# Kernel tuning notes

Measured on AMD Instinct MI355X. Metric: run time of the kernel, lower is better.

## Reference

```python
import jax, jax.numpy as jnp
import numpy as np

T, B, S, V = 50, 64, 400, 50000
D = 512; E = 512; H = 512; A = 512; POOL = 2


def setup_inputs() -> dict:
    key = jax.random.key(0)
    ks = jax.random.split(key, 20)
    def rn(k, shape, s=0.05):
        return jax.random.normal(k, shape, jnp.float32) * s
    return {
        "input_y": jax.random.randint(ks[0], (T, B), 0, V),
        "hidden": rn(ks[1], (1, B, H), 1.0),
        "context": rn(ks[2], (S, B, E), 1.0),
        "src_pad_mask": jnp.zeros((B, S), jnp.float32),
        "init_att": rn(ks[3], (B, E), 1.0),
        "coverage": jnp.zeros((B, S), jnp.float32),
        "global_ctx": rn(ks[4], (B, E), 1.0),
        "emb_W": rn(ks[5], (V, D)).at[0].set(0.0),  # padding_idx=0
        "W_ih": rn(ks[6], (3 * H, D + E)),
        "W_hh": rn(ks[7], (3 * H, H)),
        "b_ih": jnp.zeros((3 * H,), jnp.float32),
        "b_hh": jnp.zeros((3 * H,), jnp.float32),
        "W_pre": rn(ks[8], (E, A)),
        "b_pre": jnp.zeros((A,), jnp.float32),
        "W_q": rn(ks[9], (H + E, A)),
        "W_v": rn(ks[10], (A,)),
        "W_cov": rn(ks[11], (A,)),
        "W_pgen": rn(ks[12], (E + H + D,)),
        "b_pgen": jnp.zeros((), jnp.float32),
        "W_ro": rn(ks[13], (D + H + E + E, H)),
        "b_ro": jnp.zeros((H,), jnp.float32),
    }


def _gru_cell(x, h, W_ih, W_hh, b_ih, b_hh):
    # PyTorch GRUCell gate order: r, z, n
    gi = x @ W_ih.T + b_ih
    gh = h @ W_hh.T + b_hh
    i_r, i_z, i_n = jnp.split(gi, 3, axis=-1)
    h_r, h_z, h_n = jnp.split(gh, 3, axis=-1)
    r = jax.nn.sigmoid(i_r + h_r)
    z = jax.nn.sigmoid(i_z + h_z)
    n = jnp.tanh(i_n + r * h_n)
    return (1.0 - z) * n + z * h


def reference(input_y, hidden, context, src_pad_mask, init_att, coverage, global_ctx,
              emb_W, W_ih, W_hh, b_ih, b_hh, W_pre, b_pre, W_q, W_v, W_cov,
              W_pgen, b_pgen, W_ro, b_ro):
    emb = emb_W[input_y]                      # [T,B,D]
    ctx = jnp.transpose(context, (1, 0, 2))   # [B,S,E]
    precompute = ctx @ W_pre + b_pre          # [B,S,A] (computed once, as in module)
    pad = src_pad_mask > 0.5
    NEG = jnp.float32(-1e18)

    def step(carry, emb_t):
        h, cur_ctx, cov = carry
        x = jnp.concatenate([emb_t, cur_ctx], 1)          # input feed
        h0 = _gru_cell(x, h[0], W_ih, W_hh, b_ih, b_hh)   # layers=1
        h = h.at[0].set(h0)
        output = h0
        # concat attention with coverage
        q = jnp.concatenate([output, global_ctx], 1) @ W_q          # [B,A]
        tmp = jnp.tanh(precompute + q[:, None, :] + cov[..., None] * W_cov)
        energy = tmp @ W_v                                           # [B,S]
        energy = jnp.where(pad, NEG, energy)
        attn = jax.nn.softmax(energy, axis=1)
        cur_ctx = jnp.einsum('bs,bse->be', attn, ctx)
        # pointer-gen
        p_gen = jax.nn.sigmoid(
            jnp.concatenate([cur_ctx, output, emb_t], 1) @ W_pgen + b_pgen)[:, None]
        # readout + maxout (dropout is identity in eval)
        readout = jnp.concatenate([emb_t, output, cur_ctx, global_ctx], 1) @ W_ro + b_ro
        mo = readout.reshape(B, H // POOL, POOL).max(axis=-1)        # [B,H/POOL]
        cov_loss = jnp.sum(jnp.minimum(attn, cov), 1)                # cov_loss_wt=1.0
        next_cov = cov + attn
        return (h, cur_ctx, next_cov), (mo, p_gen, attn, cov_loss)

    (hidden_f, cur_ctx_f, cov_f), (g_out, g_pg, g_attn, cov_losses) = jax.lax.scan(
        step, (hidden, init_att, coverage), emb)
    return (g_out, hidden_f, g_attn[-1], cur_ctx_f, g_pg, g_attn, cov_losses, cov_f)
```

## Files before the change

kernel.cpp:

```cpp
#include <hip/hip_runtime.h>
#include <hip/hip_bf16.h>


#define T_STEPS 50
#define BB 64
#define SS 400

#define O_GOUT 0
#define O_HID 819200
#define O_ATTN_LAST 851968
#define O_CTXF 877568
#define O_PG 910336
#define O_GATTN 913536
#define O_COVL 2193536
#define O_COVF 2196736

typedef __attribute__((ext_vector_type(4))) float f4;
typedef __attribute__((ext_vector_type(8))) short s8v;
typedef __attribute__((ext_vector_type(4))) unsigned u4;

static __device__ __forceinline__ float bf2f(unsigned short u){
  unsigned v = ((unsigned)u) << 16; return __builtin_bit_cast(float, v);
}
static __device__ __forceinline__ unsigned short f2bf(float f){
  unsigned u = __builtin_bit_cast(unsigned, f);
  unsigned r = (u + 0x7FFFu + ((u >> 16) & 1u)) >> 16;
  return (unsigned short)r;
}
static __device__ __forceinline__ float sigmoidf_(float x){ return 1.f/(1.f+__expf(-x)); }
static __device__ __forceinline__ float tanhf_(float x){ float e=__expf(2.f*x); return 1.f - 2.f/(e+1.f); }
static __device__ __forceinline__ float ald32f(const float* p){
  unsigned u = __hip_atomic_load((const unsigned*)p, __ATOMIC_RELAXED, __HIP_MEMORY_SCOPE_AGENT);
  return __builtin_bit_cast(float, u);
}
static __device__ __forceinline__ void ast32f(float* p, float v){
  __hip_atomic_store((unsigned*)p, __builtin_bit_cast(unsigned, v),
                     __ATOMIC_RELAXED, __HIP_MEMORY_SCOPE_AGENT);
}

__global__ void conv_ctx(const float* __restrict__ ctx, unsigned short* __restrict__ out){
  int o = blockIdx.x*256 + threadIdx.x;
  if(o >= SS*BB*512) return;
  int e = o & 511; int b = (o>>9)&63; int s = o>>15;
  out[((b*SS+s)<<9) + e] = f2bf(ctx[o]);
}
__global__ void conv_emb(const int* __restrict__ y, const float* __restrict__ embW,
                         unsigned short* __restrict__ embU){
  int o = blockIdx.x*256+threadIdx.x; if(o>=T_STEPS*BB*512) return;
  int d = o & 511; int i = o>>9;
  embU[o] = f2bf(embW[(long)y[i]*512 + d]);
}
__global__ void conv_rest(const float* __restrict__ W_ih, const float* __restrict__ W_hh,
                          const float* __restrict__ W_pre, const float* __restrict__ W_ro,
                          const float* __restrict__ W_q,
                          const float* __restrict__ hidden, const float* __restrict__ init_att,
                          const float* __restrict__ gctx, const float* __restrict__ coverage,
                          unsigned short* __restrict__ wihbf, unsigned short* __restrict__ wpreT,
                          unsigned short* __restrict__ wroT, unsigned short* __restrict__ Wgru,
                          unsigned short* __restrict__ WqP,
                          float* __restrict__ hrow0, unsigned short* __restrict__ h0bf_init,
                          unsigned short* __restrict__ ctx0bf, float* __restrict__ gctxT,
                          float* __restrict__ cov, unsigned* __restrict__ flags){
  int o = blockIdx.x*256+threadIdx.x;
  if(o < 786432){
    int j = o>>9; int d = o&511;
    wihbf[o] = f2bf(W_ih[(long)j*1024 + d]);
  } else if(o < 1048576){
    int p = o - 786432;
    int a = p>>9; int e = p&511;
    wpreT[p] = f2bf(W_pre[(long)e*512 + a]);
  } else if(o < 2097152){
    int p = o - 1048576;
    int n = p>>11; int k = p&2047;
    wroT[p] = f2bf(W_ro[(long)k*512 + n]);
  } else if(o < 3670016){
    int p = o - 2097152;
    int rg = p >> 13; int rem = p & 8191;
    int ki = rem >> 9; int ln = (rem >> 3) & 63; int e = p & 7;
    int blk = rg/24; int r2 = rg%24; int w = r2/6; int r3 = r2%6; int g = r3>>1; int op = r3&1;
    int rl = ln & 15; int kk = ((ln>>4)<<3) + e;
    int d = blk*64 + w*16 + rl; int j = g*512 + d; int k = ki*32 + kk;
    float v = op ? W_hh[(long)j*512 + k] : W_ih[(long)j*1024 + 512 + k];
    Wgru[p] = f2bf(v);
  } else if(o < 3932160){
    int p = o - 3670016;
    int e = p&7; int ln=(p>>3)&63; int kf=(p>>9)&1; int nrg=(p>>10)&31; int blk=p>>15;
    int n = nrg*16 + (ln&15);
    int k = blk*64 + kf*32 + ((ln>>4)<<3) + e;
    WqP[p] = f2bf(W_q[(long)k*512 + n]);
  } else if(o < 4056128){
    int p = o - 3932160;
    if(p < 32768){ float v = hidden[p]; hrow0[p] = v; h0bf_init[p] = f2bf(v); }
    else if(p < 65536){ int q=p-32768; ctx0bf[q] = f2bf(init_att[q]); }
    else if(p < 98304){ int q=p-65536; int b=q>>9,e=q&511; gctxT[e*64+b]=gctx[q]; }
    else if(p < 123904){ int q=p-98304; cov[q]=coverage[q]; }
    else { int q=p-123904; if(q<64) flags[q]=0u; }
  }
}

template<int OUT_BF16>
__global__ __launch_bounds__(256) void mfma_gemm(
    const unsigned short* __restrict__ Abf, int lda,
    const unsigned short* __restrict__ Bbf, int ldb,
    void* __restrict__ Cp, int ldc, const float* __restrict__ bias, int K)
{
  __shared__ __align__(16) unsigned short Ash[128*40];
  __shared__ __align__(16) unsigned short Bsh[128*40];
  int m0 = blockIdx.x*128, n0 = blockIdx.y*128;
  int tid = threadIdx.x;
  int wid = tid>>6, lane = tid&63;
  int wm = wid>>1, wn = wid&1;
  int lr = lane&15, lg = lane>>4;
  f4 acc[4][4];
  #pragma unroll
  for(int i=0;i<4;i++)
    #pragma unroll
    for(int j=0;j<4;j++) acc[i][j]=(f4)0.f;

  for(int kt=0; kt<K; kt+=32){
    #pragma unroll
    for(int c=0;c<2;c++){
      int flat = tid*16 + c*8;
      int row = flat>>5, col = flat&31;
      const unsigned short* ga = Abf + (long)(m0+row)*lda + kt + col;
      *(uint4*)(&Ash[row*40+col]) = *(const uint4*)ga;
      const unsigned short* gb = Bbf + (long)(n0+row)*ldb + kt + col;
      *(uint4*)(&Bsh[row*40+col]) = *(const uint4*)gb;
    }
    __syncthreads();
    s8v av[4], bv[4];
    #pragma unroll
    for(int mi=0;mi<4;mi++) av[mi] = *(const s8v*)(&Ash[(wm*64+mi*16+lr)*40 + lg*8]);
    #pragma unroll
    for(int ni=0;ni<4;ni++) bv[ni] = *(const s8v*)(&Bsh[(wn*64+ni*16+lr)*40 + lg*8]);
    #pragma unroll
    for(int mi=0;mi<4;mi++)
      #pragma unroll
      for(int ni=0;ni<4;ni++)
        acc[mi][ni] = __builtin_amdgcn_mfma_f32_16x16x32_bf16(av[mi], bv[ni], acc[mi][ni], 0,0,0);
    __syncthreads();
  }
  #pragma unroll
  for(int mi=0;mi<4;mi++)
    #pragma unroll
    for(int ni=0;ni<4;ni++){
      int gc = n0 + wn*64 + ni*16 + lr;
      #pragma unroll
      for(int r=0;r<4;r++){
        int gr = m0 + wm*64 + mi*16 + lg*4 + r;
        float v = acc[mi][ni][r];
        if(bias) v += bias[gc];
        if(OUT_BF16) ((unsigned short*)Cp)[(long)gr*ldc + gc] = f2bf(v);
        else         ((float*)Cp)[(long)gr*ldc + gc] = v;
      }
    }
}

__global__ __launch_bounds__(256) void mfma_gemm_ro(
    const unsigned short* __restrict__ embU, const unsigned short* __restrict__ h0bf,
    const unsigned short* __restrict__ ctxA, const unsigned short* __restrict__ wroT,
    float* __restrict__ RO, const float* __restrict__ bias)
{
  __shared__ __align__(16) unsigned short Ash[128*40];
  __shared__ __align__(16) unsigned short Bsh[128*40];
  int m0 = blockIdx.x*128, n0 = blockIdx.y*128;
  int tid = threadIdx.x;
  int wid = tid>>6, lane = tid&63;
  int wm = wid>>1, wn = wid&1;
  int lr = lane&15, lg = lane>>4;
  f4 acc[4][4];
  #pragma unroll
  for(int i=0;i<4;i++)
    #pragma unroll
    for(int j=0;j<4;j++) acc[i][j]=(f4)0.f;

  for(int kt=0; kt<1536; kt+=32){
    const unsigned short* src = (kt<512) ? embU : (kt<1024) ? h0bf : ctxA;
    int klocal = kt & 511;
    #pragma unroll
    for(int c=0;c<2;c++){
      int flat = tid*16 + c*8;
      int row = flat>>5, col = flat&31;
      *(uint4*)(&Ash[row*40+col]) = *(const uint4*)(src + (long)(m0+row)*512 + klocal + col);
      *(uint4*)(&Bsh[row*40+col]) = *(const uint4*)(wroT + (long)(n0+row)*2048 + kt + col);
    }
    __syncthreads();
    s8v av[4], bv[4];
    #pragma unroll
    for(int mi=0;mi<4;mi++) av[mi] = *(const s8v*)(&Ash[(wm*64+mi*16+lr)*40 + lg*8]);
    #pragma unroll
    for(int ni=0;ni<4;ni++) bv[ni] = *(const s8v*)(&Bsh[(wn*64+ni*16+lr)*40 + lg*8]);
    #pragma unroll
    for(int mi=0;mi<4;mi++)
      #pragma unroll
      for(int ni=0;ni<4;ni++)
        acc[mi][ni] = __builtin_amdgcn_mfma_f32_16x16x32_bf16(av[mi], bv[ni], acc[mi][ni], 0,0,0);
    __syncthreads();
  }
  #pragma unroll
  for(int mi=0;mi<4;mi++)
    #pragma unroll
    for(int ni=0;ni<4;ni++){
      int gc = n0 + wn*64 + ni*16 + lr;
      #pragma unroll
      for(int r=0;r<4;r++){
        int gr = m0 + wm*64 + mi*16 + lg*4 + r;
        RO[(long)gr*512 + gc] = acc[mi][ni][r] + bias[gc];
      }
    }
}

__global__ __launch_bounds__(256) void small2(
  const float* __restrict__ AT, const float* __restrict__ W_q, const float* __restrict__ W_ro,
  float* __restrict__ q_g, float* __restrict__ ro_g)
{
  int blk = blockIdx.x;
  int half = blk>>7; int nblk = blk&127;
  int tid = threadIdx.x;
  int b = tid&63; int nq = tid>>6;
  int n = __builtin_amdgcn_readfirstlane(nblk*4 + nq);
  const float* W = half ? W_ro : W_q;
  int koff = half ? 1536 : 512;
  float acc = 0.f;
  const float* wp = W + (long)koff*512 + n;
  #pragma unroll 8
  for(int k=0;k<512;k++){
    acc = fmaf(AT[k*64+b], wp[(long)k*512], acc);
  }
  (half ? ro_g : q_g)[b*512+n] = acc;
}

__global__ __launch_bounds__(512) void k_step(
  const unsigned short* __restrict__ ctx0bf, float* __restrict__ ctxP,
  float* __restrict__ S_part, float* __restrict__ P_exp,
  const unsigned short* __restrict__ hprevbf,
  const float* __restrict__ hrow_in, float* __restrict__ hrow_out,
  const unsigned short* __restrict__ Wp, const unsigned short* __restrict__ WqP,
  const float* __restrict__ gi_emb, const float* __restrict__ b_hh,
  unsigned short* __restrict__ h0bf_all, float* __restrict__ qpart,
  float* __restrict__ cov, unsigned short* __restrict__ ctxA,
  const unsigned short* __restrict__ pre, const unsigned short* __restrict__ ctxbf,
  const float* __restrict__ q_g, const float* __restrict__ Wv,
  const float* __restrict__ Wcov, const float* __restrict__ padm,
  float* __restrict__ covl_part, unsigned* __restrict__ flags,
  float* __restrict__ outp, int t)
{
  __shared__ __align__(16) char smem[75008];
  const int blk = blockIdx.x;
  const int tid = threadIdx.x;
  const int w = tid>>6, lane = tid&63;
  const int lr = lane&15, lg = lane>>4;

  if(blk < 8){
    unsigned short* Ash = (unsigned short*)smem;
    unsigned short* HS  = (unsigned short*)(smem+65536);
    float* invS = (float*)(smem+74752);
    const int swz = (lr&7)<<4;
    const int rgbase = blk*24 + w*6;

    if(t>0 && tid<64){
      const float* Sp = S_part + ((t-1)&1)*256 + tid*4;
      invS[tid] = 1.f/(Sp[0]+Sp[1]+Sp[2]+Sp[3]);
    }
    __syncthreads();

    f4 acc2[6][4];
    #pragma unroll
    for(int u=0;u<6;u++)
      #pragma unroll
      for(int mi=0;mi<4;mi++) acc2[u][mi]=(f4)0.f;

    for(int kp=0; kp<2; kp++){
      for(int c = tid; c < 4096; c += 512){
        int op = c>>11; int row = (c>>5)&63; int kc = c&31;
        int e0 = kp*256 + kc*8;
        u4 v;
        if(op){
          v = *(const u4*)(hprevbf + row*512 + e0);
        } else if(t>0){
          const float* cp = ctxP + (long)row*2048 + e0;
          float sc = invS[row];
          f4 a0 = *(const f4*)(cp);
          f4 a1 = *(const f4*)(cp+512);
          f4 a2 = *(const f4*)(cp+1024);
          f4 a3 = *(const f4*)(cp+1536);
          f4 b0 = *(const f4*)(cp+4);
          f4 b1 = *(const f4*)(cp+516);
          f4 b2 = *(const f4*)(cp+1028);
          f4 b3 = *(const f4*)(cp+1540);
          f4 s0 = (a0+a1+a2+a3)*sc;
          f4 s1 = (b0+b1+b2+b3)*sc;
          v.x = (unsigned)f2bf(s0.x) | ((unsigned)f2bf(s0.y)<<16);
          v.y = (unsigned)f2bf(s0.z) | ((unsigned)f2bf(s0.w)<<16);
          v.z = (unsigned)f2bf(s1.x) | ((unsigned)f2bf(s1.y)<<16);
          v.w = (unsigned)f2bf(s1.z) | ((unsigned)f2bf(s1.w)<<16);
          if(blk == (row>>3))
            *(u4*)(ctxA + ((long)((t-1)*64+row))*512 + e0) = v;
        } else {
          v = *(const u4*)(ctx0bf + row*512 + e0);
        }
        int dst = op*32768 + row*512 + ((kc*16) ^ ((row&7)<<4));
        *(u4*)((char*)Ash + dst) = v;
      }
      __syncthreads();
      if(w<4){
        #pragma unroll 2
        for(int ktl=0; ktl<256; ktl+=32){
          s8v av[2][4];
          #pragma unroll
          for(int op=0;op<2;op++)
            #pragma unroll
            for(int mi=0;mi<4;mi++)
              av[op][mi] = *(const s8v*)((const char*)Ash + op*32768 + (mi*16+lr)*512 + ((ktl*2 + lg*16) ^ swz));
          int ki = kp*8 + (ktl>>5);
          const unsigned short* wb = Wp + (long)rgbase*8192 + ki*512 + lane*8;
          #pragma unroll
          for(int u=0;u<6;u++){
            s8v bv = *(const s8v*)(wb + (long)u*8192);
            #pragma unroll
            for(int mi=0;mi<4;mi++)
              acc2[u][mi] = __builtin_amdgcn_mfma_f32_16x16x32_bf16(av[u&1][mi], bv, acc2[u][mi], 0,0,0);
          }
        }
      }
      __syncthreads();
    }

    if(w<4){
      int d = blk*64 + w*16 + lr;
      float bhr = b_hh[d], bhz = b_hh[512+d], bhn = b_hh[1024+d];
      #pragma unroll
      for(int mi=0;mi<4;mi++){
        #pragma unroll
        for(int r=0;r<4;r++){
          int b = mi*16 + lg*4 + r;
          const float* ge = gi_emb + (long)(t*64+b)*1536;
          float g0 = __builtin_nontemporal_load(ge + d);
          float g1 = __builtin_nontemporal_load(ge + 512 + d);
          float g2 = __builtin_nontemporal_load(ge + 1024 + d);
          float rr = sigmoidf_(g0 + bhr + acc2[0][mi][r] + acc2[1][mi][r]);
          float zz = sigmoidf_(g1 + bhz + acc2[2][mi][r] + acc2[3][mi][r]);
          float nn = tanhf_(  g2       + acc2[4][mi][r] + rr*(acc2[5][mi][r] + bhn));
          float hp = hrow_in[b*512 + d];
          float hv = (1.f-zz)*nn + zz*hp;
          hrow_out[b*512+d] = hv;
          unsigned short hb = f2bf(hv);
          h0bf_all[(long)(t*64+b)*512 + d] = hb;
          HS[b*72 + w*16 + lr] = hb;
          if(t==T_STEPS-1) outp[O_HID + b*512 + d] = hv;
        }
      }
    }
    __syncthreads();
    if(w<4){
      #pragma unroll
      for(int i=0;i<8;i++){
        f4 accq[4];
        #pragma unroll
        for(int mi=0;mi<4;mi++) accq[mi]=(f4)0.f;
        #pragma unroll
        for(int kf=0;kf<2;kf++){
          s8v bv = *(const s8v*)(WqP + ((((long)blk*32 + (w*8+i))*2 + kf)*64 + lane)*8);
          #pragma unroll
          for(int mi=0;mi<4;mi++){
            s8v av = *(const s8v*)(HS + (mi*16+lr)*72 + kf*32 + lg*8);
            accq[mi] = __builtin_amdgcn_mfma_f32_16x16x32_bf16(av, bv, accq[mi], 0,0,0);
          }
        }
        int n = w*128 + i*16 + lr;
        #pragma unroll
        for(int mi=0;mi<4;mi++)
          #pragma unroll
          for(int r=0;r<4;r++)
            ast32f(qpart + (long)blk*32768 + (long)(mi*16+lg*4+r)*512 + n, accq[mi][r]);
      }
    }
    asm volatile("s_waitcnt vmcnt(0)" ::: "memory");
    __syncthreads();
    if(tid==0)
      __hip_atomic_fetch_add(flags+t, 1u, __ATOMIC_RELEASE, __HIP_MEMORY_SCOPE_AGENT);
    return;
  }

  {
    int eb = blk-8; int b = eb>>2, cq = eb&3, c0 = cq*100;
    float* q_sh  = (float*)smem;
    float* wv_sh = (float*)(smem+2048);
    float* wc_sh = (float*)(smem+4096);
    float* covL  = (float*)(smem+6144);
    float* padL  = (float*)(smem+6560);
    float* pL    = (float*)(smem+6976);
    float* red   = (float*)(smem+7392);
    float* red2  = (float*)(smem+9440);
    float* pb    = (float*)(smem+9472);

    wv_sh[tid]=Wv[tid]; wc_sh[tid]=Wcov[tid];
    if(tid<100) padL[tid]=padm[b*400+c0+tid];
    float clp = 0.f;
    if(t>0){
      const float* Sp = S_part + ((t-1)&1)*256 + b*4;
      float inv = 1.f/(Sp[0]+Sp[1]+Sp[2]+Sp[3]);
      if(tid<100){
        float p = P_exp[b*400+c0+tid]*inv;
        float co = cov[b*400+c0+tid];
        clp = fminf(p,co);
        float nc = co+p;
        cov[b*400+c0+tid]=nc;
        covL[tid]=nc;
        outp[O_GATTN + (long)(t-1)*25600 + b*400 + c0 + tid] = p;
      }
    } else {
      if(tid<100) covL[tid]=cov[b*400+c0+tid];
    }
    red[tid]=clp; __syncthreads();
    for(int o=256;o;o>>=1){ if(tid<o) red[tid]+=red[tid+o]; __syncthreads(); }
    if(t>0 && tid==0) covl_part[(long)(t-1)*256 + b*4+cq] = red[0];
    if(tid==0){
      unsigned it=0;
      while(__hip_atomic_load(flags+t, __ATOMIC_RELAXED, __HIP_MEMORY_SCOPE_AGENT) < 8u){
        __builtin_amdgcn_s_sleep(8);
        if(++it > 200000000u) break;
      }
    }
    __syncthreads();
    asm volatile("" ::: "memory");
    {
      float acc = q_g[b*512+tid];
      #pragma unroll
      for(int p=0;p<8;p++) acc += ald32f(qpart + ((long)p<<15) + b*512 + tid);
      q_sh[tid] = acc;
    }
    __syncthreads();
    float wsum = 0.f;
    for(int i=w; i<100; i+=8){
      uint4 cur = *(const uint4*)(pre + (((long)(b*400+c0+i))<<9) + lane*8);
      float cv = covL[i];
      float part = 0.f;
      const unsigned* uu = (const unsigned*)&cur;
      #pragma unroll
      for(int q4=0;q4<4;q4++){
        int a = lane*8 + q4*2;
        part += wv_sh[a]  * tanhf_(bf2f((unsigned short)(uu[q4]&0xffffu)) + q_sh[a]   + cv*wc_sh[a]);
        part += wv_sh[a+1]* tanhf_(bf2f((unsigned short)(uu[q4]>>16))    + q_sh[a+1] + cv*wc_sh[a+1]);
      }
      #pragma unroll
      for(int off=32;off;off>>=1) part += __shfl_xor(part, off, 64);
      if(lane==0){
        float e = (padL[i]>0.5f) ? -1e18f : part;
        float p = __expf(e);
        pL[i] = p;
        P_exp[b*400+c0+i] = p;
        wsum += p;
      }
    }
    if(lane==0) red2[w]=wsum;
    __syncthreads();
    if(tid==0)
      S_part[(t&1)*256 + b*4+cq] = red2[0]+red2[1]+red2[2]+red2[3]+red2[4]+red2[5]+red2[6]+red2[7];
    float acc8[8];
    #pragma unroll
    for(int j=0;j<8;j++) acc8[j]=0.f;
    for(int i=w; i<100; i+=8){
      uint4 cur = *(const uint4*)(ctxbf + (((long)(b*400+c0+i))<<9) + lane*8);
      float pv = pL[i];
      const unsigned* uu = (const unsigned*)&cur;
      acc8[0] = fmaf(pv, bf2f((unsigned short)(uu[0]&0xffffu)), acc8[0]);
      acc8[1] = fmaf(pv, bf2f((unsigned short)(uu[0]>>16)),     acc8[1]);
      acc8[2] = fmaf(pv, bf2f((unsigned short)(uu[1]&0xffffu)), acc8[2]);
      acc8[3] = fmaf(pv, bf2f((unsigned short)(uu[1]>>16)),     acc8[3]);
      acc8[4] = fmaf(pv, bf2f((unsigned short)(uu[2]&0xffffu)), acc8[4]);
      acc8[5] = fmaf(pv, bf2f((unsigned short)(uu[2]>>16)),     acc8[5]);
      acc8[6] = fmaf(pv, bf2f((unsigned short)(uu[3]&0xffffu)), acc8[6]);
      acc8[7] = fmaf(pv, bf2f((unsigned short)(uu[3]>>16)),     acc8[7]);
    }
    #pragma unroll
    for(int j=0;j<8;j++) pb[w*512 + lane*8+j] = acc8[j];
    __syncthreads();
    {
      float v = pb[tid]+pb[512+tid]+pb[1024+tid]+pb[1536+tid]
               +pb[2048+tid]+pb[2560+tid]+pb[3072+tid]+pb[3584+tid];
      ctxP[((long)b*4+cq)*512 + tid] = v;
    }
  }
}

__global__ __launch_bounds__(256) void k_fin(
  const float* __restrict__ ctxP, const float* __restrict__ S_part,
  const float* __restrict__ P_exp, const float* __restrict__ cov,
  const float* __restrict__ covl_part,
  unsigned short* __restrict__ ctxA, float* __restrict__ outp)
{
  __shared__ float red[256];
  int b = blockIdx.x; int tid = threadIdx.x;
  const int tb = T_STEPS-1;
  const float* Sp = S_part + 256 + b*4;
  float S = Sp[0]+Sp[1]+Sp[2]+Sp[3];
  float inv = 1.f/S;
  float clp;
  {
    float p = P_exp[b*400+tid]*inv;
    float co = cov[b*400+tid];
    clp = fminf(p, co);
    float nc = co+p;
    outp[O_GATTN + (long)tb*25600 + b*400 + tid] = p;
    outp[O_ATTN_LAST + b*400 + tid] = p;
    outp[O_COVF + b*400 + tid] = nc;
  }
  if(tid<144){
    int i = 256+tid;
    float p = P_exp[b*400+i]*inv;
    float co = cov[b*400+i];
    clp += fminf(p, co);
    float nc = co+p;
    outp[O_GATTN + (long)tb*25600 + b*400 + i] = p;
    outp[O_ATTN_LAST + b*400 + i] = p;
    outp[O_COVF + b*400 + i] = nc;
  }
  red[tid]=clp; __syncthreads();
  for(int o=128;o;o>>=1){ if(tid<o) red[tid]+=red[tid+o]; __syncthreads(); }
  if(tid==0) outp[O_COVL + tb*64 + b] = red[0];
  if(tid<49){
    const float* cp = covl_part + (long)tid*256 + b*4;
    outp[O_COVL + tid*64 + b] = cp[0]+cp[1]+cp[2]+cp[3];
  }
  for(int c=tid;c<512;c+=256){
    float v = (ctxP[(long)b*2048+c]+ctxP[(long)b*2048+512+c]
              +ctxP[(long)b*2048+1024+c]+ctxP[(long)b*2048+1536+c])*inv;
    outp[O_CTXF + b*512 + c] = v;
    ctxA[(long)(tb*64+b)*512 + c] = f2bf(v);
  }
}

__global__ __launch_bounds__(256) void k_post(
  const unsigned short* __restrict__ embU, const unsigned short* __restrict__ h0bf,
  const unsigned short* __restrict__ ctxA, const float* __restrict__ Wpg,
  const float* __restrict__ bpg, const float* __restrict__ RO,
  const float* __restrict__ ro_g, float* __restrict__ outp)
{
  int blk = blockIdx.x;
  if(blk < 800){
    int wid = threadIdx.x>>6, lane=threadIdx.x&63;
    int m = blk*4 + wid;
    float acc=0.f;
    #pragma unroll
    for(int i=0;i<8;i++){
      int k = i*64+lane;
      acc = fmaf(bf2f(ctxA[(long)m*512+k]), Wpg[k], acc);
      acc = fmaf(bf2f(h0bf[(long)m*512+k]), Wpg[512+k], acc);
      acc = fmaf(bf2f(embU[(long)m*512+k]), Wpg[1024+k], acc);
    }
    #pragma unroll
    for(int off=32; off; off>>=1) acc += __shfl_xor(acc, off, 64);
    if(lane==0) outp[O_PG + m] = sigmoidf_(acc + bpg[0]);
  } else {
    int o = (blk-800)*256 + threadIdx.x;
    int h = o & 255; int m = o>>8; int b = m & 63;
    float v0 = RO[(long)m*512 + 2*h]   + ro_g[b*512 + 2*h];
    float v1 = RO[(long)m*512 + 2*h+1] + ro_g[b*512 + 2*h+1];
    outp[O_GOUT + o] = fmaxf(v0,v1);
  }
}

extern "C" void kernel_launch(void* const* d_in, const int* in_sizes, int n_in,
                              void* d_out, int out_size, void* d_ws, size_t ws_size,
                              hipStream_t stream)
{
  (void)in_sizes; (void)n_in; (void)out_size; (void)ws_size;
  const int*   y       = (const int*)d_in[0];
  const float* hidden  = (const float*)d_in[1];
  const float* context = (const float*)d_in[2];
  const float* padm    = (const float*)d_in[3];
  const float* init_att= (const float*)d_in[4];
  const float* coverage= (const float*)d_in[5];
  const float* gctx    = (const float*)d_in[6];
  const float* embW    = (const float*)d_in[7];
  const float* W_ih    = (const float*)d_in[8];
  const float* W_hh    = (const float*)d_in[9];
  const float* b_ih    = (const float*)d_in[10];
  const float* b_hh    = (const float*)d_in[11];
  const float* W_pre   = (const float*)d_in[12];
  const float* b_pre   = (const float*)d_in[13];
  const float* W_q     = (const float*)d_in[14];
  const float* W_v     = (const float*)d_in[15];
  const float* W_cov   = (const float*)d_in[16];
  const float* W_pg    = (const float*)d_in[17];
  const float* b_pg    = (const float*)d_in[18];
  const float* W_ro    = (const float*)d_in[19];
  const float* b_ro    = (const float*)d_in[20];
  float* out = (float*)d_out;

  char* wsb = (char*)d_ws;
  size_t off = 0;
  auto alloc = [&](size_t bytes)->char*{ char* p = wsb+off; off += (bytes+255)&~255UL; return p; };
  unsigned short* pre    = (unsigned short*)alloc(25600UL*512*2);
  unsigned short* ctxbf  = (unsigned short*)alloc(13107200UL*2);
  unsigned short* embU   = (unsigned short*)alloc(3200UL*512*2);
  unsigned short* wihbf  = (unsigned short*)alloc(1536UL*512*2);
  unsigned short* wpreT  = (unsigned short*)alloc(512UL*512*2);
  unsigned short* wroT   = (unsigned short*)alloc(512UL*2048*2);
  unsigned short* Wgru   = (unsigned short*)alloc(192UL*8192*2);
  unsigned short* WqP    = (unsigned short*)alloc(262144UL*2);
  float* gi_emb = (float*)alloc(3200UL*1536*4);
  float* RO     = (float*)alloc(3200UL*512*4);
  float* q_g    = (float*)alloc(64UL*512*4);
  float* ro_g   = (float*)alloc(64UL*512*4);
  float* hrow0  = (float*)alloc(64UL*512*4);
  float* hrow1  = (float*)alloc(64UL*512*4);
  float* gctxT  = (float*)alloc(512UL*64*4);
  unsigned short* h0bf = (unsigned short*)alloc(3200UL*512*2);
  unsigned short* h0bf_init = (unsigned short*)alloc(64UL*512*2);
  unsigned short* ctx0bf    = (unsigned short*)alloc(64UL*512*2);
  unsigned short* ctxA = (unsigned short*)alloc(3200UL*512*2);
  float* ctxP   = (float*)alloc(64UL*4*512*4);
  float* P_exp  = (float*)alloc(64UL*400*4);
  float* S_part = (float*)alloc(2UL*256*4);
  float* qpart  = (float*)alloc(8UL*64*512*4);
  float* cov    = (float*)alloc(64UL*400*4);
  float* covl_part = (float*)alloc(50UL*256*4);
  unsigned* flags = (unsigned*)alloc(64UL*4);

  conv_ctx <<<dim3(51200),dim3(256),0,stream>>>(context, ctxbf);
  conv_emb <<<dim3(6400), dim3(256),0,stream>>>(y, embW, embU);
  conv_rest<<<dim3(15845),dim3(256),0,stream>>>(W_ih, W_hh, W_pre, W_ro, W_q,
                                                hidden, init_att, gctx, coverage,
                                                wihbf, wpreT, wroT, Wgru, WqP,
                                                hrow0, h0bf_init, ctx0bf, gctxT, cov, flags);

  mfma_gemm<1><<<dim3(200,4),dim3(256),0,stream>>>(ctxbf,512, wpreT,512,  pre,   512, b_pre, 512);
  mfma_gemm<0><<<dim3(25,12),dim3(256),0,stream>>>(embU, 512, wihbf,512,  gi_emb,1536, b_ih, 512);
  small2<<<dim3(256),dim3(256),0,stream>>>(gctxT, W_q, W_ro, q_g, ro_g);

  for(int t=0; t<T_STEPS; t++){
    float* hin  = (t&1) ? hrow1 : hrow0;
    float* hout = (t&1) ? hrow0 : hrow1;
    const unsigned short* hprevbf = t ? (h0bf + (long)(t-1)*32768) : h0bf_init;
    k_step<<<dim3(264),dim3(512),0,stream>>>(ctx0bf, ctxP, S_part, P_exp, hprevbf,
                                             hin, hout, Wgru, WqP, gi_emb, b_hh,
                                             h0bf, qpart, cov, ctxA, pre, ctxbf,
                                             q_g, W_v, W_cov, padm, covl_part,
                                             flags, out, t);
  }

  k_fin<<<dim3(64),dim3(256),0,stream>>>(ctxP, S_part, P_exp, cov, covl_part, ctxA, out);
  mfma_gemm_ro<<<dim3(25,4),dim3(256),0,stream>>>(embU, h0bf, ctxA, wroT, RO, b_ro);
  k_post<<<dim3(4000),dim3(256),0,stream>>>(embU, h0bf, ctxA, W_pg, b_pg, RO, ro_g, out);
}
```

Before: 3.131 ms.

## Split GRU MFMA work across all 8 waves and prefetch attention rows before spin-wait

The GRU blocks now use all 8 waves instead of 4, with each wave taking half the batch rows for the recurrent and query MFMAs. This halves the per-wave serial MFMA chain on the critical path. The attention blocks issue loads of their precompute and context rows into registers before spin-waiting on the GRU flag, so memory latency overlaps the wait. The score and weighted-context loops are fused into one pass that uses the shuffled-broadcast probability instead of a shared-memory round trip. In exchange, register pressure rises (26 u4 vectors held across the wait), which may reduce occupancy or cause spills.

```diff
diff --git a/kernel.cpp b/kernel.cpp
--- a/kernel.cpp
+++ b/kernel.cpp
@@ -256,7 +256,8 @@
     unsigned short* HS  = (unsigned short*)(smem+65536);
     float* invS = (float*)(smem+74752);
     const int swz = (lr&7)<<4;
-    const int rgbase = blk*24 + w*6;
+    const int dg = w&3, bh = w>>2;
+    const int rgbase = blk*24 + dg*6;
 
     if(t>0 && tid<64){
       const float* Sp = S_part + ((t-1)&1)*256 + tid*4;
@@ -264,11 +265,11 @@
     }
     __syncthreads();
 
-    f4 acc2[6][4];
+    f4 acc2[6][2];
     #pragma unroll
     for(int u=0;u<6;u++)
       #pragma unroll
-      for(int mi=0;mi<4;mi++) acc2[u][mi]=(f4)0.f;
+      for(int mm=0;mm<2;mm++) acc2[u][mm]=(f4)0.f;
 
     for(int kp=0; kp<2; kp++){
       for(int c = tid; c < 4096; c += 512){
@@ -303,34 +304,37 @@
         *(u4*)((char*)Ash + dst) = v;
       }
       __syncthreads();
-      if(w<4){
+      {
         #pragma unroll 2
         for(int ktl=0; ktl<256; ktl+=32){
-          s8v av[2][4];
+          s8v av[2][2];
           #pragma unroll
           for(int op=0;op<2;op++)
             #pragma unroll
-            for(int mi=0;mi<4;mi++)
-              av[op][mi] = *(const s8v*)((const char*)Ash + op*32768 + (mi*16+lr)*512 + ((ktl*2 + lg*16) ^ swz));
+            for(int mm=0;mm<2;mm++){
+              int mi = bh*2+mm;
+              av[op][mm] = *(const s8v*)((const char*)Ash + op*32768 + (mi*16+lr)*512 + ((ktl*2 + lg*16) ^ swz));
+            }
           int ki = kp*8 + (ktl>>5);
           const unsigned short* wb = Wp + (long)rgbase*8192 + ki*512 + lane*8;
           #pragma unroll
           for(int u=0;u<6;u++){
             s8v bv = *(const s8v*)(wb + (long)u*8192);
             #pragma unroll
-            for(int mi=0;mi<4;mi++)
-              acc2[u][mi] = __builtin_amdgcn_mfma_f32_16x16x32_bf16(av[u&1][mi], bv, acc2[u][mi], 0,0,0);
+            for(int mm=0;mm<2;mm++)
+              acc2[u][mm] = __builtin_amdgcn_mfma_f32_16x16x32_bf16(av[u&1][mm], bv, acc2[u][mm], 0,0,0);
           }
         }
       }
       __syncthreads();
     }
 
-    if(w<4){
-      int d = blk*64 + w*16 + lr;
+    {
+      int d = blk*64 + dg*16 + lr;
       float bhr = b_hh[d], bhz = b_hh[512+d], bhn = b_hh[1024+d];
       #pragma unroll
-      for(int mi=0;mi<4;mi++){
+      for(int mm=0;mm<2;mm++){
+        int mi = bh*2+mm;
         #pragma unroll
         for(int r=0;r<4;r++){
           int b = mi*16 + lg*4 + r;
@@ -338,41 +342,41 @@
           float g0 = __builtin_nontemporal_load(ge + d);
           float g1 = __builtin_nontemporal_load(ge + 512 + d);
           float g2 = __builtin_nontemporal_load(ge + 1024 + d);
-          float rr = sigmoidf_(g0 + bhr + acc2[0][mi][r] + acc2[1][mi][r]);
-          float zz = sigmoidf_(g1 + bhz + acc2[2][mi][r] + acc2[3][mi][r]);
-          float nn = tanhf_(  g2       + acc2[4][mi][r] + rr*(acc2[5][mi][r] + bhn));
+          float rr = sigmoidf_(g0 + bhr + acc2[0][mm][r] + acc2[1][mm][r]);
+          float zz = sigmoidf_(g1 + bhz + acc2[2][mm][r] + acc2[3][mm][r]);
+          float nn = tanhf_(  g2       + acc2[4][mm][r] + rr*(acc2[5][mm][r] + bhn));
           float hp = hrow_in[b*512 + d];
           float hv = (1.f-zz)*nn + zz*hp;
           hrow_out[b*512+d] = hv;
           unsigned short hb = f2bf(hv);
           h0bf_all[(long)(t*64+b)*512 + d] = hb;
-          HS[b*72 + w*16 + lr] = hb;
+          HS[b*72 + dg*16 + lr] = hb;
           if(t==T_STEPS-1) outp[O_HID + b*512 + d] = hv;
         }
       }
     }
     __syncthreads();
-    if(w<4){
+    {
       #pragma unroll
       for(int i=0;i<8;i++){
-        f4 accq[4];
-        #pragma unroll
-        for(int mi=0;mi<4;mi++) accq[mi]=(f4)0.f;
+        f4 accq[2];
+        accq[0]=(f4)0.f; accq[1]=(f4)0.f;
         #pragma unroll
         for(int kf=0;kf<2;kf++){
-          s8v bv = *(const s8v*)(WqP + ((((long)blk*32 + (w*8+i))*2 + kf)*64 + lane)*8);
+          s8v bv = *(const s8v*)(WqP + ((((long)blk*32 + (dg*8+i))*2 + kf)*64 + lane)*8);
           #pragma unroll
-          for(int mi=0;mi<4;mi++){
+          for(int mm=0;mm<2;mm++){
+            int mi = bh*2+mm;
             s8v av = *(const s8v*)(HS + (mi*16+lr)*72 + kf*32 + lg*8);
-            accq[mi] = __builtin_amdgcn_mfma_f32_16x16x32_bf16(av, bv, accq[mi], 0,0,0);
+            accq[mm] = __builtin_amdgcn_mfma_f32_16x16x32_bf16(av, bv, accq[mm], 0,0,0);
           }
         }
-        int n = w*128 + i*16 + lr;
+        int n = dg*128 + i*16 + lr;
         #pragma unroll
-        for(int mi=0;mi<4;mi++)
+        for(int mm=0;mm<2;mm++)
           #pragma unroll
           for(int r=0;r<4;r++)
-            ast32f(qpart + (long)blk*32768 + (long)(mi*16+lg*4+r)*512 + n, accq[mi][r]);
+            ast32f(qpart + (long)blk*32768 + (long)((bh*2+mm)*16+lg*4+r)*512 + n, accq[mm][r]);
       }
     }
     asm volatile("s_waitcnt vmcnt(0)" ::: "memory");
@@ -389,7 +393,6 @@
     float* wc_sh = (float*)(smem+4096);
     float* covL  = (float*)(smem+6144);
     float* padL  = (float*)(smem+6560);
-    float* pL    = (float*)(smem+6976);
     float* red   = (float*)(smem+7392);
     float* red2  = (float*)(smem+9440);
     float* pb    = (float*)(smem+9472);
@@ -412,6 +415,16 @@
     } else {
       if(tid<100) covL[tid]=cov[b*400+c0+tid];
     }
+    const unsigned short* prow = pre   + (((long)(b*400+c0))<<9) + lane*8;
+    const unsigned short* crow = ctxbf + (((long)(b*400+c0))<<9) + lane*8;
+    u4 pr[13], cr[13];
+    #pragma unroll
+    for(int j=0;j<13;j++){
+      int i = w + j*8;
+      long ro = (long)((i<100)? i : 0) << 9;
+      pr[j] = *(const u4*)(prow + ro);
+      cr[j] = *(const u4*)(crow + ro);
+    }
     red[tid]=clp; __syncthreads();
     for(int o=256;o;o>>=1){ if(tid<o) red[tid]+=red[tid+o]; __syncthreads(); }
     if(t>0 && tid==0) covl_part[(long)(t-1)*256 + b*4+cq] = red[0];
@@ -432,47 +445,45 @@
     }
     __syncthreads();
     float wsum = 0.f;
-    for(int i=w; i<100; i+=8){
-      uint4 cur = *(const uint4*)(pre + (((long)(b*400+c0+i))<<9) + lane*8);
-      float cv = covL[i];
-      float part = 0.f;
-      const unsigned* uu = (const unsigned*)&cur;
-      #pragma unroll
-      for(int q4=0;q4<4;q4++){
-        int a = lane*8 + q4*2;
-        part += wv_sh[a]  * tanhf_(bf2f((unsigned short)(uu[q4]&0xffffu)) + q_sh[a]   + cv*wc_sh[a]);
-        part += wv_sh[a+1]* tanhf_(bf2f((unsigned short)(uu[q4]>>16))    + q_sh[a+1] + cv*wc_sh[a+1]);
-      }
-      #pragma unroll
-      for(int off=32;off;off>>=1) part += __shfl_xor(part, off, 64);
-      if(lane==0){
+    float acc8[8];
+    #pragma unroll
+    for(int j=0;j<8;j++) acc8[j]=0.f;
+    #pragma unroll
+    for(int j=0;j<13;j++){
+      int i = w + j*8;
+      if(i<100){
+        u4 cur = pr[j];
+        const unsigned* uu = (const unsigned*)&cur;
+        float cv = covL[i];
+        float part = 0.f;
+        #pragma unroll
+        for(int q4=0;q4<4;q4++){
+          int a = lane*8 + q4*2;
+          part += wv_sh[a]  * tanhf_(bf2f((unsigned short)(uu[q4]&0xffffu)) + q_sh[a]   + cv*wc_sh[a]);
+          part += wv_sh[a+1]* tanhf_(bf2f((unsigned short)(uu[q4]>>16))    + q_sh[a+1] + cv*wc_sh[a+1]);
+        }
+        #pragma unroll
+        for(int off=32;off;off>>=1) part += __shfl_xor(part, off, 64);
         float e = (padL[i]>0.5f) ? -1e18f : part;
         float p = __expf(e);
-        pL[i] = p;
-        P_exp[b*400+c0+i] = p;
+        if(lane==0) P_exp[b*400+c0+i] = p;
         wsum += p;
+        u4 cc = cr[j];
+        const unsigned* cu = (const unsigned*)&cc;
+        acc8[0] = fmaf(p, bf2f((unsigned short)(cu[0]&0xffffu)), acc8[0]);
+        acc8[1] = fmaf(p, bf2f((unsigned short)(cu[0]>>16)),     acc8[1]);
+        acc8[2] = fmaf(p, bf2f((unsigned short)(cu[1]&0xffffu)), acc8[2]);
+        acc8[3] = fmaf(p, bf2f((unsigned short)(cu[1]>>16)),     acc8[3]);
+        acc8[4] = fmaf(p, bf2f((unsigned short)(cu[2]&0xffffu)), acc8[4]);
+        acc8[5] = fmaf(p, bf2f((unsigned short)(cu[2]>>16)),     acc8[5]);
+        acc8[6] = fmaf(p, bf2f((unsigned short)(cu[3]&0xffffu)), acc8[6]);
+        acc8[7] = fmaf(p, bf2f((unsigned short)(cu[3]>>16)),     acc8[7]);
       }
     }
     if(lane==0) red2[w]=wsum;
     __syncthreads();
     if(tid==0)
       S_part[(t&1)*256 + b*4+cq] = red2[0]+red2[1]+red2[2]+red2[3]+red2[4]+red2[5]+red2[6]+red2[7];
-    float acc8[8];
-    #pragma unroll
-    for(int j=0;j<8;j++) acc8[j]=0.f;
-    for(int i=w; i<100; i+=8){
-      uint4 cur = *(const uint4*)(ctxbf + (((long)(b*400+c0+i))<<9) + lane*8);
-      float pv = pL[i];
-      const unsigned* uu = (const unsigned*)&cur;
-      acc8[0] = fmaf(pv, bf2f((unsigned short)(uu[0]&0xffffu)), acc8[0]);
-      acc8[1] = fmaf(pv, bf2f((unsigned short)(uu[0]>>16)),     acc8[1]);
-      acc8[2] = fmaf(pv, bf2f((unsigned short)(uu[1]&0xffffu)), acc8[2]);
-      acc8[3] = fmaf(pv, bf2f((unsigned short)(uu[1]>>16)),     acc8[3]);
-      acc8[4] = fmaf(pv, bf2f((unsigned short)(uu[2]&0xffffu)), acc8[4]);
-      acc8[5] = fmaf(pv, bf2f((unsigned short)(uu[2]>>16)),     acc8[5]);
-      acc8[6] = fmaf(pv, bf2f((unsigned short)(uu[3]&0xffffu)), acc8[6]);
-      acc8[7] = fmaf(pv, bf2f((unsigned short)(uu[3]>>16)),     acc8[7]);
-    }
     #pragma unroll
     for(int j=0;j<8;j++) pb[w*512 + lane*8+j] = acc8[j];
     __syncthreads();
```

Measured after the change: 2.779 ms. 1.13x faster.
